# Performance work log

Hardware: AMD Instinct MI355X
Metric: run time of the kernel (lower is better)

The kernel has to match this reference:

```python
import jax, jax.numpy as jnp
import numpy as np

W_KERNEL = 5      # dilation kernel size (w)
K_BG = 0.1        # background weight (k)
RELAX = 5.0       # sigmoid temperature (relax)
INF = 1e4         # 'no zero in column' sentinel (>> image diagonal)
EPS = 1e-7        # DiceLoss eps


def setup_inputs() -> dict:
    key = jax.random.key(0)
    k1, k2 = jax.random.split(key)
    B, H, W = 32, 256, 256
    preds = jax.random.normal(k1, (B, H, W), dtype=jnp.float32)
    targets = (jax.random.uniform(k2, (B, H, W)) > 0.99).astype(jnp.float32)
    return {"preds": preds, "targets": targets}


def _dilate(t, w):
    # cv2.dilate with w x w ones kernel == sliding-window max, SAME padding
    pad = w // 2
    return jax.lax.reduce_window(t, -jnp.inf, jax.lax.max,
                                 (1, w, w), (1, 1, 1),
                                 [(0, 0), (pad, pad), (pad, pad)])


def _vertical_dist(zero_mask):
    # per-column distance (in rows) to nearest zero pixel; [B,H,W] -> [B,H,W]
    B, H, W = zero_mask.shape
    rows = jnp.moveaxis(zero_mask, 1, 0)  # [H,B,W]

    def step(carry, z):
        d = jnp.where(z, 0.0, jnp.minimum(carry + 1.0, INF))
        return d, d

    init = jnp.full((B, W), INF, dtype=jnp.float32)
    _, fwd = jax.lax.scan(step, init, rows)
    _, bwd = jax.lax.scan(step, init, rows[::-1])
    g = jnp.minimum(fwd, bwd[::-1])  # [H,B,W]
    return jnp.moveaxis(g, 0, 1)


def _edt(fat):
    # exact euclidean distance transform (distance to nearest zero pixel),
    # separable two-pass: vertical 1D distance, then horizontal min-plus.
    B, H, W = fat.shape
    g = _vertical_dist(fat == 0)  # [B,H,W]
    col = jnp.arange(W, dtype=jnp.float32)
    off2 = (col[:, None] - col[None, :]) ** 2  # [W_j, W_k]

    def per_img(gi):  # gi: [H,W]
        # d2[i,j] = min_k g[i,k]^2 + (j-k)^2   -> [H,W,W] intermediate
        d2 = jnp.min(gi[:, None, :] ** 2 + off2[None, :, :], axis=-1)
        return jnp.sqrt(d2)

    return jax.lax.map(per_img, g)  # sequential over batch caps memory


def _distance_maps(targets):
    fat = _dilate(targets, W_KERNEL)          # [B,H,W]
    d = _edt(fat)                              # [B,H,W]
    soft = jax.nn.sigmoid(d / RELAX)
    soft = soft - jnp.min(soft, axis=(1, 2), keepdims=True)
    mx = jnp.max(soft, axis=(1, 2), keepdims=True)
    soft = soft / jnp.where(mx > 0, mx, 1.0)
    dm_soft = soft + (1.0 - fat) * K_BG
    has_fg = jnp.max(targets, axis=(1, 2), keepdims=True) > 0
    return jnp.where(has_fg, dm_soft, 1.0 - targets)


def reference(preds, targets):
    p = jax.nn.sigmoid(preds)
    dm = jax.lax.stop_gradient(_distance_maps(targets))  # computed in numpy in torch => constant
    pw = p * dm
    bs = pw.shape[0]
    y_pred = pw.reshape(bs, 1, -1)
    y_true = targets.reshape(bs, 1, -1)
    # smp DiceLoss('binary', from_logits=False): dims=(0,2), smooth=0, eps=1e-7
    inter = jnp.sum(y_pred * y_true, axis=(0, 2))
    card = jnp.sum(y_pred + y_true, axis=(0, 2))
    dice = (2.0 * inter) / jnp.maximum(card, EPS)
    loss = 1.0 - dice
    mask = (jnp.sum(y_true, axis=(0, 2)) > 0).astype(loss.dtype)
    return jnp.mean(loss * mask)
```

## Files before the change

kernel.cpp:

```cpp
#include <hip/hip_runtime.h>
#include <math.h>

#define BB 32
#define HH 256
#define WW 256
#define HW (HH*WW)
#define TOT (BB*HW)
#define K_BG 0.1f
#define RELAX 5.0f
#define EPS_D 1e-7
#define NBF 2048

typedef unsigned long long u64;
typedef unsigned short u16;

__device__ __forceinline__ float sigf(float x) { return 1.0f / (1.0f + expf(-x)); }

__global__ void k_maskdil(const float* __restrict__ tg, u64* __restrict__ dmask) {
    __shared__ u64 nz[12][4];
    __shared__ u64 hd[12][4];
    int blk = blockIdx.x;
    int b = blk >> 5, band = blk & 31;
    int r0 = band * 8;
    int t = threadIdx.x, w = t >> 6;
    const float* img = tg + b * HW;
    for (int rr = 0; rr < 12; ++rr) {
        int rg = r0 + rr - 2;
        float v = (rg >= 0 && rg < HH) ? img[rg * WW + t] : 0.0f;
        u64 bal = __ballot(v != 0.0f);
        if ((t & 63) == 0) nz[rr][w] = bal;
    }
    __syncthreads();
    if (t < 48) {
        int rr = t >> 2, k = t & 3;
        u64 m = nz[rr][k];
        u64 ml = (k > 0) ? nz[rr][k - 1] : 0ULL;
        u64 mr = (k < 3) ? nz[rr][k + 1] : 0ULL;
        hd[rr][k] = m | (m << 1) | (m << 2) | (m >> 1) | (m >> 2)
                  | (ml >> 62) | (ml >> 63) | (mr << 62) | (mr << 63);
    }
    __syncthreads();
    if (t < 32) {
        int rr = t >> 2, k = t & 3;
        u64 o = hd[rr][k] | hd[rr + 1][k] | hd[rr + 2][k] | hd[rr + 3][k] | hd[rr + 4][k];
        dmask[b * 1024 + (r0 + rr) * 4 + k] = o;
    }
}

__global__ __launch_bounds__(256) void k_edt(const u64* __restrict__ dmask,
                                             float* __restrict__ d,
                                             float* __restrict__ rowmn,
                                             float* __restrict__ rowmx) {
    __shared__ u64 mk[1024];
    __shared__ u16 gS[WW];
    __shared__ float smn[4], smx[4];
    int row = blockIdx.x;
    int b = row >> 8, i = row & 255;
    int t = threadIdx.x;
    const uint4* src4 = (const uint4*)(dmask + b * 1024);
    uint4* mk4 = (uint4*)mk;
    mk4[t] = src4[t];
    mk4[t + 256] = src4[t + 256];
    __syncthreads();

    int j = t, w = j >> 6;
    u64 bitm = 1ULL << (j & 63);
    int g0 = 0;
    if (mk[i * 4 + w] & bitm) {
        int up = 10000;
        for (int k = 1; k <= i; ++k)
            if (!(mk[(i - k) * 4 + w] & bitm)) { up = k; break; }
        int dn = 10000;
        for (int k = 1; k < HH - i; ++k)
            if (!(mk[(i + k) * 4 + w] & bitm)) { dn = k; break; }
        g0 = min(up, dn);
    }
    gS[j] = (u16)g0;
    __syncthreads();

    float gv = (float)g0;
    float best = gv * gv;
    for (int r = 1; r < WW; ++r) {
        float rr = (float)(r * r);
        if (rr >= best) break;
        int jl = j - r, jr = j + r;
        if (jl >= 0) { float v = (float)gS[jl]; best = fminf(best, v * v + rr); }
        if (jr < WW) { float v = (float)gS[jr]; best = fminf(best, v * v + rr); }
    }
    float dv = sqrtf(best);
    d[(long)row * WW + j] = dv;

    float mn = dv, mx = dv;
    for (int off = 32; off > 0; off >>= 1) {
        mn = fminf(mn, __shfl_down(mn, off, 64));
        mx = fmaxf(mx, __shfl_down(mx, off, 64));
    }
    int wid = t >> 6, lane = t & 63;
    if (lane == 0) { smn[wid] = mn; smx[wid] = mx; }
    __syncthreads();
    if (t == 0) {
        float a = smn[0], z = smx[0];
        for (int k = 1; k < 4; ++k) { a = fminf(a, smn[k]); z = fmaxf(z, smx[k]); }
        rowmn[row] = a; rowmx[row] = z;
    }
}

__global__ void k_mnmx(const float* __restrict__ rowmn, const float* __restrict__ rowmx,
                       float* __restrict__ dmnb, float* __restrict__ dmxb) {
    int b = blockIdx.x, t = threadIdx.x;
    float mn = rowmn[b * HH + t], mx = rowmx[b * HH + t];
    for (int off = 32; off > 0; off >>= 1) {
        mn = fminf(mn, __shfl_down(mn, off, 64));
        mx = fmaxf(mx, __shfl_down(mx, off, 64));
    }
    __shared__ float smn[4], smx[4];
    int wid = t >> 6, lane = t & 63;
    if (lane == 0) { smn[wid] = mn; smx[wid] = mx; }
    __syncthreads();
    if (t == 0) {
        float a = smn[0], z = smx[0];
        for (int k = 1; k < 4; ++k) { a = fminf(a, smn[k]); z = fmaxf(z, smx[k]); }
        dmnb[b] = a; dmxb[b] = z;
    }
}

__global__ void k_final(const float4* __restrict__ preds4, const float4* __restrict__ tg4,
                        const u64* __restrict__ dmask, const float4* __restrict__ d4,
                        const float* __restrict__ dmnb, const float* __restrict__ dmxb,
                        float2* __restrict__ part) {
    int tid = blockIdx.x * blockDim.x + threadIdx.x;
    int idx = tid << 2;
    int b = idx / HW;
    float4 p = preds4[tid], tv = tg4[tid], dd = d4[tid];
    u64 mword = dmask[idx >> 6];
    int sh = idx & 63;
    float pe[4] = {p.x, p.y, p.z, p.w};
    float te[4] = {tv.x, tv.y, tv.z, tv.w};
    float de[4] = {dd.x, dd.y, dd.z, dd.w};
    float dmx = dmxb[b];
    float inter = 0.0f, card = 0.0f;
    if (dmx > 0.0f) {
        float smin = sigf(dmnb[b] / RELAX);
        float smax = sigf(dmx / RELAX);
        float m = smax - smin;
        float denom = (m > 0.0f) ? m : 1.0f;
        #pragma unroll
        for (int e = 0; e < 4; ++e) {
            float fat = (float)((mword >> (sh + e)) & 1ULL);
            float soft = (sigf(de[e] / RELAX) - smin) / denom;
            float dm = soft + (1.0f - fat) * K_BG;
            float pw = sigf(pe[e]) * dm;
            inter += pw * te[e];
            card += pw + te[e];
        }
    } else {
        #pragma unroll
        for (int e = 0; e < 4; ++e) {
            float dm = 1.0f - te[e];
            float pw = sigf(pe[e]) * dm;
            inter += pw * te[e];
            card += pw + te[e];
        }
    }
    for (int off = 32; off > 0; off >>= 1) {
        inter += __shfl_down(inter, off, 64);
        card  += __shfl_down(card,  off, 64);
    }
    __shared__ float si[4], sc[4];
    int wid = threadIdx.x >> 6, lane = threadIdx.x & 63;
    if (lane == 0) { si[wid] = inter; sc[wid] = card; }
    __syncthreads();
    if (threadIdx.x == 0) {
        float ti = 0.0f, tc = 0.0f;
        for (int i = 0; i < 4; ++i) { ti += si[i]; tc += sc[i]; }
        part[blockIdx.x] = make_float2(ti, tc);
    }
}

__global__ void k_fin(const float2* __restrict__ part, const float* __restrict__ dmxb,
                      float* __restrict__ out) {
    int t = threadIdx.x;
    double di = 0.0, dc = 0.0;
    for (int i = t; i < NBF; i += 256) { di += (double)part[i].x; dc += (double)part[i].y; }
    for (int off = 32; off > 0; off >>= 1) {
        di += __shfl_down(di, off, 64);
        dc += __shfl_down(dc, off, 64);
    }
    __shared__ double sdi[4], sdc[4];
    int wid = t >> 6, lane = t & 63;
    if (lane == 0) { sdi[wid] = di; sdc[wid] = dc; }
    __syncthreads();
    if (t == 0) {
        double I = 0.0, C = 0.0;
        for (int i = 0; i < 4; ++i) { I += sdi[i]; C += sdc[i]; }
        int any = 0;
        for (int b = 0; b < BB; ++b) any |= (dmxb[b] > 0.0f);
        double dice = 2.0 * I / fmax(C, (double)EPS_D);
        out[0] = any ? (float)(1.0 - dice) : 0.0f;
    }
}

extern "C" void kernel_launch(void* const* d_in, const int* in_sizes, int n_in,
                              void* d_out, int out_size, void* d_ws, size_t ws_size,
                              hipStream_t stream) {
    const float* preds = (const float*)d_in[0];
    const float* tg    = (const float*)d_in[1];
    float* out = (float*)d_out;

    float* darr = (float*)d_ws;
    u64* dmask  = (u64*)(darr + TOT);
    float2* part = (float2*)(dmask + BB * 1024);
    float* rowmn = (float*)(part + NBF);
    float* rowmx = rowmn + BB * HH;
    float* dmnb  = rowmx + BB * HH;
    float* dmxb  = dmnb + BB;

    hipLaunchKernelGGL(k_maskdil, dim3(BB * 32), dim3(WW), 0, stream, tg, dmask);
    hipLaunchKernelGGL(k_edt, dim3(BB * HH), dim3(WW), 0, stream, dmask, darr, rowmn, rowmx);
    hipLaunchKernelGGL(k_mnmx, dim3(BB), dim3(HH), 0, stream, rowmn, rowmx, dmnb, dmxb);
    hipLaunchKernelGGL(k_final, dim3(NBF), dim3(256), 0, stream,
                       (const float4*)preds, (const float4*)tg, dmask, (const float4*)darr,
                       dmnb, dmxb, part);
    hipLaunchKernelGGL(k_fin, dim3(1), dim3(256), 0, stream, part, dmxb, out);
}
```

Baseline: 104.7 us.

## Fuse EDT with dice partial sums via linear decomposition of normalized weights

The per-image min-max normalisation is affine, so the dice intersection and cardinality are rewritten as linear combinations of per-pixel partial sums (sp*sd*t, sp*t, sp*sd, sp, sp*(1-fat), t) that can be accumulated before the image min/max is known. This lets the EDT kernel also read preds and targets, compute the sigmoids and reduce all eight statistics per row. The distance map is no longer written to memory, and the separate full-image final pass and one launch are removed. The dilation kernel also processes 16-row bands instead of 8. In exchange the float sums are reordered, which changes rounding slightly, and the EDT kernel does more reduction work per block.

```diff
diff --git a/kernel.cpp b/kernel.cpp
--- a/kernel.cpp
+++ b/kernel.cpp
@@ -9,7 +9,6 @@
 #define K_BG 0.1f
 #define RELAX 5.0f
 #define EPS_D 1e-7
-#define NBF 2048
 
 typedef unsigned long long u64;
 typedef unsigned short u16;
@@ -17,21 +16,21 @@
 __device__ __forceinline__ float sigf(float x) { return 1.0f / (1.0f + expf(-x)); }
 
 __global__ void k_maskdil(const float* __restrict__ tg, u64* __restrict__ dmask) {
-    __shared__ u64 nz[12][4];
-    __shared__ u64 hd[12][4];
+    __shared__ u64 nz[20][4];
+    __shared__ u64 hd[20][4];
     int blk = blockIdx.x;
-    int b = blk >> 5, band = blk & 31;
-    int r0 = band * 8;
+    int b = blk >> 4, band = blk & 15;
+    int r0 = band * 16;
     int t = threadIdx.x, w = t >> 6;
     const float* img = tg + b * HW;
-    for (int rr = 0; rr < 12; ++rr) {
+    for (int rr = 0; rr < 20; ++rr) {
         int rg = r0 + rr - 2;
         float v = (rg >= 0 && rg < HH) ? img[rg * WW + t] : 0.0f;
         u64 bal = __ballot(v != 0.0f);
         if ((t & 63) == 0) nz[rr][w] = bal;
     }
     __syncthreads();
-    if (t < 48) {
+    if (t < 80) {
         int rr = t >> 2, k = t & 3;
         u64 m = nz[rr][k];
         u64 ml = (k > 0) ? nz[rr][k - 1] : 0ULL;
@@ -40,23 +39,28 @@
                   | (ml >> 62) | (ml >> 63) | (mr << 62) | (mr << 63);
     }
     __syncthreads();
-    if (t < 32) {
+    if (t < 64) {
         int rr = t >> 2, k = t & 3;
         u64 o = hd[rr][k] | hd[rr + 1][k] | hd[rr + 2][k] | hd[rr + 3][k] | hd[rr + 4][k];
         dmask[b * 1024 + (r0 + rr) * 4 + k] = o;
     }
 }
 
-__global__ __launch_bounds__(256) void k_edt(const u64* __restrict__ dmask,
-                                             float* __restrict__ d,
-                                             float* __restrict__ rowmn,
-                                             float* __restrict__ rowmx) {
+__global__ __launch_bounds__(256) void k_mega(const float* __restrict__ preds,
+                                              const float* __restrict__ tg,
+                                              const u64* __restrict__ dmask,
+                                              float4* __restrict__ part1,
+                                              float4* __restrict__ part2) {
     __shared__ u64 mk[1024];
     __shared__ u16 gS[WW];
-    __shared__ float smn[4], smx[4];
+    __shared__ float red[8][4];
     int row = blockIdx.x;
     int b = row >> 8, i = row & 255;
     int t = threadIdx.x;
+
+    float p  = preds[row * WW + t];
+    float tv = tg[row * WW + t];
+
     const uint4* src4 = (const uint4*)(dmask + b * 1024);
     uint4* mk4 = (uint4*)mk;
     mk4[t] = src4[t];
@@ -65,8 +69,9 @@
 
     int j = t, w = j >> 6;
     u64 bitm = 1ULL << (j & 63);
+    int fgbit = (mk[i * 4 + w] & bitm) ? 1 : 0;
     int g0 = 0;
-    if (mk[i * 4 + w] & bitm) {
+    if (fgbit) {
         int up = 10000;
         for (int k = 1; k <= i; ++k)
             if (!(mk[(i - k) * 4 + w] & bitm)) { up = k; break; }
@@ -88,113 +93,96 @@
         if (jr < WW) { float v = (float)gS[jr]; best = fminf(best, v * v + rr); }
     }
     float dv = sqrtf(best);
-    d[(long)row * WW + j] = dv;
-
-    float mn = dv, mx = dv;
+
+    float sp = sigf(p);
+    float sd = sigf(dv / RELAX);
+    float vals[8];
+    vals[0] = sp * sd * tv;
+    vals[1] = sp * tv;
+    vals[2] = sp * sd;
+    vals[3] = sp;
+    vals[4] = sp * (1.0f - (float)fgbit);
+    vals[5] = tv;
+    vals[6] = dv;
+    vals[7] = dv;
     for (int off = 32; off > 0; off >>= 1) {
-        mn = fminf(mn, __shfl_down(mn, off, 64));
-        mx = fmaxf(mx, __shfl_down(mx, off, 64));
+        #pragma unroll
+        for (int q = 0; q < 6; ++q) vals[q] += __shfl_down(vals[q], off, 64);
+        vals[6] = fminf(vals[6], __shfl_down(vals[6], off, 64));
+        vals[7] = fmaxf(vals[7], __shfl_down(vals[7], off, 64));
     }
     int wid = t >> 6, lane = t & 63;
-    if (lane == 0) { smn[wid] = mn; smx[wid] = mx; }
+    if (lane == 0) {
+        #pragma unroll
+        for (int q = 0; q < 8; ++q) red[q][wid] = vals[q];
+    }
     __syncthreads();
     if (t == 0) {
-        float a = smn[0], z = smx[0];
-        for (int k = 1; k < 4; ++k) { a = fminf(a, smn[k]); z = fmaxf(z, smx[k]); }
-        rowmn[row] = a; rowmx[row] = z;
-    }
-}
-
-__global__ void k_mnmx(const float* __restrict__ rowmn, const float* __restrict__ rowmx,
-                       float* __restrict__ dmnb, float* __restrict__ dmxb) {
+        float s[8];
+        #pragma unroll
+        for (int q = 0; q < 6; ++q) s[q] = red[q][0] + red[q][1] + red[q][2] + red[q][3];
+        s[6] = fminf(fminf(red[6][0], red[6][1]), fminf(red[6][2], red[6][3]));
+        s[7] = fmaxf(fmaxf(red[7][0], red[7][1]), fmaxf(red[7][2], red[7][3]));
+        part1[row] = make_float4(s[0], s[1], s[2], s[3]);
+        part2[row] = make_float4(s[4], s[5], s[6], s[7]);
+    }
+}
+
+__global__ void k_img(const float4* __restrict__ part1, const float4* __restrict__ part2,
+                      float4* __restrict__ imgout) {
+    __shared__ float red[8][4];
     int b = blockIdx.x, t = threadIdx.x;
-    float mn = rowmn[b * HH + t], mx = rowmx[b * HH + t];
+    float4 p1 = part1[b * HH + t];
+    float4 p2 = part2[b * HH + t];
+    float vals[8] = {p1.x, p1.y, p1.z, p1.w, p2.x, p2.y, p2.z, p2.w};
     for (int off = 32; off > 0; off >>= 1) {
-        mn = fminf(mn, __shfl_down(mn, off, 64));
-        mx = fmaxf(mx, __shfl_down(mx, off, 64));
-    }
-    __shared__ float smn[4], smx[4];
+        #pragma unroll
+        for (int q = 0; q < 6; ++q) vals[q] += __shfl_down(vals[q], off, 64);
+        vals[6] = fminf(vals[6], __shfl_down(vals[6], off, 64));
+        vals[7] = fmaxf(vals[7], __shfl_down(vals[7], off, 64));
+    }
     int wid = t >> 6, lane = t & 63;
-    if (lane == 0) { smn[wid] = mn; smx[wid] = mx; }
+    if (lane == 0) {
+        #pragma unroll
+        for (int q = 0; q < 8; ++q) red[q][wid] = vals[q];
+    }
     __syncthreads();
     if (t == 0) {
-        float a = smn[0], z = smx[0];
-        for (int k = 1; k < 4; ++k) { a = fminf(a, smn[k]); z = fmaxf(z, smx[k]); }
-        dmnb[b] = a; dmxb[b] = z;
-    }
-}
-
-__global__ void k_final(const float4* __restrict__ preds4, const float4* __restrict__ tg4,
-                        const u64* __restrict__ dmask, const float4* __restrict__ d4,
-                        const float* __restrict__ dmnb, const float* __restrict__ dmxb,
-                        float2* __restrict__ part) {
-    int tid = blockIdx.x * blockDim.x + threadIdx.x;
-    int idx = tid << 2;
-    int b = idx / HW;
-    float4 p = preds4[tid], tv = tg4[tid], dd = d4[tid];
-    u64 mword = dmask[idx >> 6];
-    int sh = idx & 63;
-    float pe[4] = {p.x, p.y, p.z, p.w};
-    float te[4] = {tv.x, tv.y, tv.z, tv.w};
-    float de[4] = {dd.x, dd.y, dd.z, dd.w};
-    float dmx = dmxb[b];
-    float inter = 0.0f, card = 0.0f;
-    if (dmx > 0.0f) {
-        float smin = sigf(dmnb[b] / RELAX);
-        float smax = sigf(dmx / RELAX);
-        float m = smax - smin;
-        float denom = (m > 0.0f) ? m : 1.0f;
-        #pragma unroll
-        for (int e = 0; e < 4; ++e) {
-            float fat = (float)((mword >> (sh + e)) & 1ULL);
-            float soft = (sigf(de[e] / RELAX) - smin) / denom;
-            float dm = soft + (1.0f - fat) * K_BG;
-            float pw = sigf(pe[e]) * dm;
-            inter += pw * te[e];
-            card += pw + te[e];
+        float A  = red[0][0] + red[0][1] + red[0][2] + red[0][3];
+        float Bs = red[1][0] + red[1][1] + red[1][2] + red[1][3];
+        float Ap = red[2][0] + red[2][1] + red[2][2] + red[2][3];
+        float Bp = red[3][0] + red[3][1] + red[3][2] + red[3][3];
+        float Cp = red[4][0] + red[4][1] + red[4][2] + red[4][3];
+        float T  = red[5][0] + red[5][1] + red[5][2] + red[5][3];
+        float dmn = fminf(fminf(red[6][0], red[6][1]), fminf(red[6][2], red[6][3]));
+        float dmx = fmaxf(fmaxf(red[7][0], red[7][1]), fmaxf(red[7][2], red[7][3]));
+        float inter, card, any;
+        if (dmx > 0.0f) {
+            float smin = sigf(dmn / RELAX);
+            float smax = sigf(dmx / RELAX);
+            float m = smax - smin;
+            float denom = (m > 0.0f) ? m : 1.0f;
+            inter = (A - smin * Bs) / denom;
+            card  = (Ap - smin * Bp) / denom + K_BG * Cp + T;
+            any = 1.0f;
+        } else {
+            inter = 0.0f;
+            card = Bp - Bs + T;
+            any = 0.0f;
         }
-    } else {
-        #pragma unroll
-        for (int e = 0; e < 4; ++e) {
-            float dm = 1.0f - te[e];
-            float pw = sigf(pe[e]) * dm;
-            inter += pw * te[e];
-            card += pw + te[e];
+        imgout[b] = make_float4(inter, card, any, 0.0f);
+    }
+}
+
+__global__ void k_fin(const float4* __restrict__ imgout, float* __restrict__ out) {
+    if (threadIdx.x == 0) {
+        double I = 0.0, C = 0.0;
+        int any = 0;
+        for (int b = 0; b < BB; ++b) {
+            float4 v = imgout[b];
+            I += (double)v.x; C += (double)v.y;
+            any |= (v.z > 0.0f);
         }
-    }
-    for (int off = 32; off > 0; off >>= 1) {
-        inter += __shfl_down(inter, off, 64);
-        card  += __shfl_down(card,  off, 64);
-    }
-    __shared__ float si[4], sc[4];
-    int wid = threadIdx.x >> 6, lane = threadIdx.x & 63;
-    if (lane == 0) { si[wid] = inter; sc[wid] = card; }
-    __syncthreads();
-    if (threadIdx.x == 0) {
-        float ti = 0.0f, tc = 0.0f;
-        for (int i = 0; i < 4; ++i) { ti += si[i]; tc += sc[i]; }
-        part[blockIdx.x] = make_float2(ti, tc);
-    }
-}
-
-__global__ void k_fin(const float2* __restrict__ part, const float* __restrict__ dmxb,
-                      float* __restrict__ out) {
-    int t = threadIdx.x;
-    double di = 0.0, dc = 0.0;
-    for (int i = t; i < NBF; i += 256) { di += (double)part[i].x; dc += (double)part[i].y; }
-    for (int off = 32; off > 0; off >>= 1) {
-        di += __shfl_down(di, off, 64);
-        dc += __shfl_down(dc, off, 64);
-    }
-    __shared__ double sdi[4], sdc[4];
-    int wid = t >> 6, lane = t & 63;
-    if (lane == 0) { sdi[wid] = di; sdc[wid] = dc; }
-    __syncthreads();
-    if (t == 0) {
-        double I = 0.0, C = 0.0;
-        for (int i = 0; i < 4; ++i) { I += sdi[i]; C += sdc[i]; }
-        int any = 0;
-        for (int b = 0; b < BB; ++b) any |= (dmxb[b] > 0.0f);
         double dice = 2.0 * I / fmax(C, (double)EPS_D);
         out[0] = any ? (float)(1.0 - dice) : 0.0f;
     }
@@ -207,19 +195,14 @@
     const float* tg    = (const float*)d_in[1];
     float* out = (float*)d_out;
 
-    float* darr = (float*)d_ws;
-    u64* dmask  = (u64*)(darr + TOT);
-    float2* part = (float2*)(dmask + BB * 1024);
-    float* rowmn = (float*)(part + NBF);
-    float* rowmx = rowmn + BB * HH;
-    float* dmnb  = rowmx + BB * HH;
-    float* dmxb  = dmnb + BB;
-
-    hipLaunchKernelGGL(k_maskdil, dim3(BB * 32), dim3(WW), 0, stream, tg, dmask);
-    hipLaunchKernelGGL(k_edt, dim3(BB * HH), dim3(WW), 0, stream, dmask, darr, rowmn, rowmx);
-    hipLaunchKernelGGL(k_mnmx, dim3(BB), dim3(HH), 0, stream, rowmn, rowmx, dmnb, dmxb);
-    hipLaunchKernelGGL(k_final, dim3(NBF), dim3(256), 0, stream,
-                       (const float4*)preds, (const float4*)tg, dmask, (const float4*)darr,
-                       dmnb, dmxb, part);
-    hipLaunchKernelGGL(k_fin, dim3(1), dim3(256), 0, stream, part, dmxb, out);
-}
+    u64* dmask   = (u64*)d_ws;
+    float4* part1 = (float4*)(dmask + BB * 1024);
+    float4* part2 = part1 + BB * HH;
+    float4* imgout = part2 + BB * HH;
+
+    hipLaunchKernelGGL(k_maskdil, dim3(BB * 16), dim3(WW), 0, stream, tg, dmask);
+    hipLaunchKernelGGL(k_mega, dim3(BB * HH), dim3(WW), 0, stream, preds, tg, dmask,
+                       part1, part2);
+    hipLaunchKernelGGL(k_img, dim3(BB), dim3(HH), 0, stream, part1, part2, imgout);
+    hipLaunchKernelGGL(k_fin, dim3(1), dim3(64), 0, stream, imgout, out);
+}
```

After: 103.1 us. Within noise of the previous version (-1.5%).
